# Kernel tuning notes

Hardware: AMD Instinct MI355X
Metric: run time of the kernel (lower is better)

## Reference

```python
import jax, jax.numpy as jnp
import numpy as np
import math

NUM_HEADS = 8
EPS = 1e-12  # torch F.normalize eps


def setup_inputs() -> dict:
    key = jax.random.key(0)
    ks = jax.random.split(key, 11)
    b, t, l, c = 2, 8, 1024, 256
    s = 0.02
    return {
        "q": jax.random.normal(ks[0], (b, t, l, c), jnp.float32),
        "k": jax.random.normal(ks[1], (b, t, l, c), jnp.float32),
        "v": jax.random.normal(ks[2], (b, t, l, c), jnp.float32),
        "Wq": jax.random.normal(ks[3], (c, c), jnp.float32) * s,
        "bq": jax.random.normal(ks[4], (c,), jnp.float32) * s,
        "Wk": jax.random.normal(ks[5], (c, c), jnp.float32) * s,
        "bk": jax.random.normal(ks[6], (c,), jnp.float32) * s,
        "Wv": jax.random.normal(ks[7], (c, c), jnp.float32) * s,
        "bv": jax.random.normal(ks[8], (c,), jnp.float32) * s,
        "Wm": jax.random.normal(ks[9], (c, c), jnp.float32) * s,
        "bm": jax.random.normal(ks[10], (c,), jnp.float32) * s,
    }


def _proj_norm(x, W, bias, h, d):
    # Linear (torch: x @ W.T + b), split heads, L2-normalize over head_dim.
    b_, t_, l_, c_ = x.shape
    y = (x @ W.T + bias).reshape(b_, t_, l_, h, d).transpose(0, 1, 3, 2, 4)  # [b,t,h,l,d]
    n = jnp.maximum(jnp.linalg.norm(y, axis=-1, keepdims=True), EPS)
    return y / n


def reference(q, k, v, Wq, bq, Wk, bk, Wv, bv, Wm, bm):
    b, t, l, c = q.shape
    h = NUM_HEADS
    d = c // h
    shortcut = q
    qn = _proj_norm(q, Wq, bq, h, d)  # [b,t,h,l,d]
    kn = _proj_norm(k, Wk, bk, h, d)
    vn = _proj_norm(v, Wv, bv, h, d)
    scores = jnp.einsum('bthqd,bthkd->bthqk', qn, kn) / math.sqrt(d)
    attn = jax.nn.softmax(scores, axis=-1)
    x = jnp.einsum('bthqk,bthkd->bthqd', attn, vn)  # [b,t,h,l,d]
    x = x.transpose(0, 1, 3, 2, 4).reshape(b, t, l, c)
    return x @ Wm.T + bm + shortcut
```

## Files before the change

### kernel.cpp

```cpp
#include <hip/hip_runtime.h>
#include <hip/hip_bf16.h>


#define NTOK  16384
#define CDIM  256
#define LSEQ  1024
#define HEADS 8
#define DHEAD 32

typedef _Float16 f16;
typedef __attribute__((ext_vector_type(2))) _Float16 f16x2;
typedef __attribute__((ext_vector_type(4))) _Float16 f16x4;
typedef __attribute__((ext_vector_type(8))) _Float16 f16x8;
typedef __attribute__((ext_vector_type(4))) float f32x4;
typedef __attribute__((ext_vector_type(16))) float f32x16;

#define QSCALE (0.17677669529663687f * 1.4426950408889634f)

__device__ __forceinline__ f16x2 pkcvt(float a, float b) {
  auto r = __builtin_amdgcn_cvt_pkrtz(a, b);
  union { decltype(r) in; f16x2 out; } u;
  u.in = r;
  return u.out;
}

__device__ __forceinline__ f16x4 pack4(float4 a) {
  union { f16x4 v; f16x2 h[2]; } u;
  u.h[0] = pkcvt(a.x, a.y);
  u.h[1] = pkcvt(a.z, a.w);
  return u.v;
}

__global__ __launch_bounds__(256)
void cvt_w_kernel(const float* __restrict__ Wq, const float* __restrict__ Wk,
                  const float* __restrict__ Wv, const float* __restrict__ Wm,
                  f16* __restrict__ dst) {
  const int m = blockIdx.x >> 6;
  const float* src = (m == 0) ? Wq : (m == 1) ? Wk : (m == 2) ? Wv : Wm;
  const int base = (blockIdx.x & 63) * 1024 + threadIdx.x * 4;
  const int och = base >> 8, ch = base & 255;
  float4 a = *(const float4*)(src + base);
  *(f16x4*)(dst + m * 65536 + (ch >> 5) * 8192 + och * 32 + (ch & 31)) =
      pack4(a);
}

#define PKKB 1288

__global__ __launch_bounds__(256, 2)
void proj_mfma_kernel(const float* __restrict__ xq, const float* __restrict__ xk,
                      const float* __restrict__ xv, const f16* __restrict__ w16,
                      const float* __restrict__ bq, const float* __restrict__ bk,
                      const float* __restrict__ bv,
                      f16* __restrict__ qn, f16* __restrict__ kn,
                      f16* __restrict__ vt) {
  __shared__ f16 xl[8 * PKKB];
  const int which = blockIdx.y;
  const float* x    = (which == 0) ? xq : (which == 1) ? xk : xv;
  const float* bias = (which == 0) ? bq : (which == 1) ? bk : bv;
  const f16* W      = w16 + which * 65536;
  f16* out          = (which == 0) ? qn : (which == 1) ? kn : vt;
  const float scale = (which == 0) ? QSCALE : 1.0f;
  const bool transposed = (which == 2);

  const int tid = threadIdx.x;
  const int wave = tid >> 6, lane = tid & 63;
  const int quad = lane >> 4, l16 = lane & 15;
  const int tokbase = blockIdx.x * 32;
  const int wbase = wave * 64;

  {
    const int c16 = lane;
#pragma unroll
    for (int r = 0; r < 8; ++r) {
      const int tok = r * 4 + wave;
      float4 a = *(const float4*)(x + (size_t)(tokbase + tok) * CDIM + c16 * 4);
      *(f16x4*)(&xl[(c16 >> 3) * PKKB + tok * 40 + (c16 & 7) * 4]) = pack4(a);
    }
  }
  __syncthreads();

  f32x4 acc[4][2];
#pragma unroll
  for (int mt = 0; mt < 4; ++mt)
#pragma unroll
    for (int nt = 0; nt < 2; ++nt) acc[mt][nt] = (f32x4){0.f, 0.f, 0.f, 0.f};

#pragma unroll
  for (int kk = 0; kk < 8; ++kk) {
    f16x8 af[4];
#pragma unroll
    for (int mt = 0; mt < 4; ++mt)
      af[mt] = *(const f16x8*)(W + kk * 8192 + (wbase + mt * 16 + l16) * 32 +
                               quad * 8);
    f16x8 bf0 = *(const f16x8*)(&xl[kk * PKKB + l16 * 40 + quad * 8]);
    f16x8 bf1 = *(const f16x8*)(&xl[kk * PKKB + (16 + l16) * 40 + quad * 8]);
#pragma unroll
    for (int mt = 0; mt < 4; ++mt) {
      acc[mt][0] = __builtin_amdgcn_mfma_f32_16x16x32_f16(af[mt], bf0,
                                                          acc[mt][0], 0, 0, 0);
      acc[mt][1] = __builtin_amdgcn_mfma_f32_16x16x32_f16(af[mt], bf1,
                                                          acc[mt][1], 0, 0, 0);
    }
  }

  const int bt = tokbase >> 10, l0 = tokbase & 1023;
#pragma unroll
  for (int hh = 0; hh < 2; ++hh) {
    const int h = wave * 2 + hh;
    const size_t hb = (size_t)(bt * HEADS + h) * (LSEQ * DHEAD);
    float4 b0 = *(const float4*)(bias + wbase + hh * 32 + quad * 4);
    float4 b1 = *(const float4*)(bias + wbase + hh * 32 + 16 + quad * 4);
#pragma unroll
    for (int nt = 0; nt < 2; ++nt) {
      f32x4 a0 = acc[hh * 2 + 0][nt];
      f32x4 a1 = acc[hh * 2 + 1][nt];
      float v0[4], v1[4];
      v0[0] = a0[0] + b0.x; v0[1] = a0[1] + b0.y;
      v0[2] = a0[2] + b0.z; v0[3] = a0[3] + b0.w;
      v1[0] = a1[0] + b1.x; v1[1] = a1[1] + b1.y;
      v1[2] = a1[2] + b1.z; v1[3] = a1[3] + b1.w;
      float ss = 0.f;
#pragma unroll
      for (int r = 0; r < 4; ++r) ss += v0[r] * v0[r] + v1[r] * v1[r];
      ss += __shfl_xor(ss, 16);
      ss += __shfl_xor(ss, 32);
      const float inv = scale / fmaxf(sqrtf(ss), 1e-12f);
      const int tok_l = l0 + nt * 16 + l16;
      if (!transposed) {
        f16x4 o0, o1;
#pragma unroll
        for (int r = 0; r < 4; ++r) {
          o0[r] = (f16)(v0[r] * inv);
          o1[r] = (f16)(v1[r] * inv);
        }
        *(f16x4*)(out + hb + (size_t)tok_l * DHEAD + quad * 4) = o0;
        *(f16x4*)(out + hb + (size_t)tok_l * DHEAD + 16 + quad * 4) = o1;
      } else {
        const int tcol = (tok_l & ~12) | ((tok_l & 4) << 1) | ((tok_l & 8) >> 1);
#pragma unroll
        for (int r = 0; r < 4; ++r) {
          out[hb + (size_t)(quad * 4 + r) * LSEQ + tcol] = (f16)(v0[r] * inv);
          out[hb + (size_t)(16 + quad * 4 + r) * LSEQ + tcol] = (f16)(v1[r] * inv);
        }
      }
    }
  }
}

#define TKROW 40
#define TVROW 136

__global__ __launch_bounds__(256, 4)
void attn_mfma_kernel(const f16* __restrict__ qn,
                      const f16* __restrict__ kn,
                      const f16* __restrict__ vt,
                      f16* __restrict__ xo) {
  __shared__ f16 kl[2][128 * TKROW];
  __shared__ f16 vl[2][32 * TVROW];
  const int tid  = threadIdx.x;
  const int wave = tid >> 6, lane = tid & 63;
  const int l32 = lane & 31, hi = lane >> 5;
  const int wid = (blockIdx.x & 7) * 128 + (blockIdx.x >> 3);
  const int bth = wid >> 3;
  const int qbase = ((wid & 7) << 7) + wave * 32;
  const size_t hb = (size_t)bth * (LSEQ * DHEAD);

  const f16* qp = qn + hb + (size_t)(qbase + l32) * DHEAD + hi * 8;
  const f16x8 qf0 = *(const f16x8*)qp;
  const f16x8 qf1 = *(const f16x8*)(qp + 16);

  const int krow_w = wave * 32 + (lane >> 1), kc0 = (lane & 1) * 16;
  const f16* gKb = kn + hb + (size_t)krow_w * DHEAD + kc0;
  const int lK = krow_w * TKROW + kc0;
  const int vrow_w = wave * 8 + (lane >> 3), vc0 = (lane & 7) * 8;
  const f16* gVb = vt + hb + (size_t)vrow_w * LSEQ + vc0;
  const int lV = vrow_w * TVROW + vc0;

  f32x16 oacc, z16;
#pragma unroll
  for (int r = 0; r < 16; ++r) { oacc[r] = 0.f; z16[r] = 0.f; }
  float ls0 = 0.f, ls1 = 0.f;

#define EXPPV(s, v0, v1) { \
    union { f16x8 v; f16x2 h[4]; } _q0, _q1; \
    _Pragma("unroll") \
    for (int i = 0; i < 4; ++i) { \
      float e0 = __builtin_amdgcn_exp2f(s[2 * i]); \
      float e1 = __builtin_amdgcn_exp2f(s[2 * i + 1]); \
      ls0 += e0; ls1 += e1; \
      _q0.h[i] = pkcvt(e0, e1); \
      float e2 = __builtin_amdgcn_exp2f(s[8 + 2 * i]); \
      float e3 = __builtin_amdgcn_exp2f(s[9 + 2 * i]); \
      ls0 += e2; ls1 += e3; \
      _q1.h[i] = pkcvt(e2, e3); \
    } \
    oacc = __builtin_amdgcn_mfma_f32_32x32x16_f16(v0, _q0.v, oacc, 0, 0, 0); \
    oacc = __builtin_amdgcn_mfma_f32_32x32x16_f16(v1, _q1.v, oacc, 0, 0, 0); }

  f16x8 gk0 = *(const f16x8*)gKb;
  f16x8 gk1 = *(const f16x8*)(gKb + 8);
  f16x8 gv0 = *(const f16x8*)gVb;
  f16x8 gv1 = *(const f16x8*)(gVb + 64);
  *(f16x8*)(&kl[0][lK])      = gk0;
  *(f16x8*)(&kl[0][lK + 8])  = gk1;
  *(f16x8*)(&vl[0][lV])      = gv0;
  *(f16x8*)(&vl[0][lV + 64]) = gv1;
  gk0 = *(const f16x8*)(gKb + 128 * DHEAD);
  gk1 = *(const f16x8*)(gKb + 128 * DHEAD + 8);
  gv0 = *(const f16x8*)(gVb + 128);
  gv1 = *(const f16x8*)(gVb + 128 + 64);
  __syncthreads();

  for (int t = 0; t < 8; ++t) {
    const f16* kb = kl[t & 1];
    const f16* vb = vl[t & 1];
    __builtin_amdgcn_s_setprio(1);
#pragma unroll
    for (int sub = 0; sub < 4; ++sub) {
      f16x8 kf0 = *(const f16x8*)(kb + (sub * 32 + l32) * TKROW + hi * 8);
      f16x8 kf1 = *(const f16x8*)(kb + (sub * 32 + l32) * TKROW + hi * 8 + 16);
      f16x8 vf0 = *(const f16x8*)(vb + l32 * TVROW + sub * 32 + hi * 8);
      f16x8 vf1 = *(const f16x8*)(vb + l32 * TVROW + sub * 32 + hi * 8 + 16);
      f32x16 s = __builtin_amdgcn_mfma_f32_32x32x16_f16(kf0, qf0, z16, 0, 0, 0);
      s = __builtin_amdgcn_mfma_f32_32x32x16_f16(kf1, qf1, s, 0, 0, 0);
      EXPPV(s, vf0, vf1)
    }
    __builtin_amdgcn_s_setprio(0);
    if (t < 7) {
      __syncthreads();
      *(f16x8*)(&kl[(t + 1) & 1][lK])      = gk0;
      *(f16x8*)(&kl[(t + 1) & 1][lK + 8])  = gk1;
      *(f16x8*)(&vl[(t + 1) & 1][lV])      = gv0;
      *(f16x8*)(&vl[(t + 1) & 1][lV + 64]) = gv1;
      if (t < 6) {
        gk0 = *(const f16x8*)(gKb + (size_t)(t + 2) * 128 * DHEAD);
        gk1 = *(const f16x8*)(gKb + (size_t)(t + 2) * 128 * DHEAD + 8);
        gv0 = *(const f16x8*)(gVb + (t + 2) * 128);
        gv1 = *(const f16x8*)(gVb + (t + 2) * 128 + 64);
      }
      __syncthreads();
    }
  }
#undef EXPPV

  float lsum = ls0 + ls1;
  lsum += __shfl_xor(lsum, 32);
  const float inv = __builtin_amdgcn_rcpf(lsum);

  f16* op = xo + hb + (size_t)(qbase + l32) * DHEAD + hi * 4;
#pragma unroll
  for (int g = 0; g < 4; ++g) {
    union { f16x4 v; f16x2 h[2]; } o;
    o.h[0] = pkcvt(oacc[4 * g + 0] * inv, oacc[4 * g + 1] * inv);
    o.h[1] = pkcvt(oacc[4 * g + 2] * inv, oacc[4 * g + 3] * inv);
    *(f16x4*)(op + 8 * g) = o.v;
  }
}

#define OKKB 1288

__global__ __launch_bounds__(256, 2)
void out_proj_mfma_kernel(const f16* __restrict__ xatt,
                          const f16* __restrict__ wm16,
                          const float* __restrict__ bm,
                          const float* __restrict__ resid,
                          float* __restrict__ out) {
  __shared__ f16 xl[8 * OKKB];
  const int tid = threadIdx.x;
  const int wave = tid >> 6, lane = tid & 63;
  const int quad = lane >> 4, l16 = lane & 15;
  const int tokbase = blockIdx.x * 32;
  const int wbase = wave * 64;
  const int bt = tokbase >> 10, l0 = tokbase & 1023;

  {
#pragma unroll
    for (int r = 0; r < 4; ++r) {
      const int flat = r * 256 + tid;
      const int kk = flat >> 7, rem = flat & 127;
      const int tok = rem >> 2, c8 = rem & 3;
      const f16* gp = xatt + (size_t)(bt * HEADS + kk) * (LSEQ * DHEAD) +
                      (size_t)(l0 + tok) * DHEAD + c8 * 8;
      *(f16x8*)(&xl[kk * OKKB + tok * 40 + c8 * 8]) = *(const f16x8*)gp;
    }
  }
  __syncthreads();

  f32x4 acc[4][2];
#pragma unroll
  for (int mt = 0; mt < 4; ++mt)
#pragma unroll
    for (int nt = 0; nt < 2; ++nt) acc[mt][nt] = (f32x4){0.f, 0.f, 0.f, 0.f};

#pragma unroll
  for (int kk = 0; kk < 8; ++kk) {
    f16x8 af[4];
#pragma unroll
    for (int mt = 0; mt < 4; ++mt)
      af[mt] = *(const f16x8*)(wm16 + kk * 8192 +
                               (wbase + mt * 16 + l16) * 32 + quad * 8);
    f16x8 bf0 = *(const f16x8*)(&xl[kk * OKKB + l16 * 40 + quad * 8]);
    f16x8 bf1 = *(const f16x8*)(&xl[kk * OKKB + (16 + l16) * 40 + quad * 8]);
#pragma unroll
    for (int mt = 0; mt < 4; ++mt) {
      acc[mt][0] = __builtin_amdgcn_mfma_f32_16x16x32_f16(af[mt], bf0,
                                                          acc[mt][0], 0, 0, 0);
      acc[mt][1] = __builtin_amdgcn_mfma_f32_16x16x32_f16(af[mt], bf1,
                                                          acc[mt][1], 0, 0, 0);
    }
  }

#pragma unroll
  for (int mt = 0; mt < 4; ++mt) {
    float4 bv = *(const float4*)(bm + wbase + mt * 16 + quad * 4);
#pragma unroll
    for (int nt = 0; nt < 2; ++nt) {
      const int tok = tokbase + nt * 16 + l16;
      const size_t off = (size_t)tok * CDIM + wbase + mt * 16 + quad * 4;
      float4 rv = *(const float4*)(resid + off);
      float4 o;
      o.x = acc[mt][nt][0] + bv.x + rv.x;
      o.y = acc[mt][nt][1] + bv.y + rv.y;
      o.z = acc[mt][nt][2] + bv.z + rv.z;
      o.w = acc[mt][nt][3] + bv.w + rv.w;
      *(float4*)(out + off) = o;
    }
  }
}

extern "C" void kernel_launch(void* const* d_in, const int* in_sizes, int n_in,
                              void* d_out, int out_size, void* d_ws,
                              size_t ws_size, hipStream_t stream) {
  const float* q  = (const float*)d_in[0];
  const float* k  = (const float*)d_in[1];
  const float* v  = (const float*)d_in[2];
  const float* Wq = (const float*)d_in[3];
  const float* bq = (const float*)d_in[4];
  const float* Wk = (const float*)d_in[5];
  const float* bk = (const float*)d_in[6];
  const float* Wv = (const float*)d_in[7];
  const float* bv = (const float*)d_in[8];
  const float* Wm = (const float*)d_in[9];
  const float* bm = (const float*)d_in[10];
  float* outp = (float*)d_out;

  f16* ws = (f16*)d_ws;
  const size_t TENS = (size_t)NTOK * CDIM;
  f16* qn  = ws;
  f16* kn  = ws + TENS;
  f16* vt  = ws + 2 * TENS;
  f16* w16 = ws + 3 * TENS;
  f16* xa  = qn;

  dim3 blk(256);
  cvt_w_kernel<<<dim3(256), blk, 0, stream>>>(Wq, Wk, Wv, Wm, w16);
  proj_mfma_kernel<<<dim3(512, 3), blk, 0, stream>>>(q, k, v, w16, bq, bk, bv,
                                                     qn, kn, vt);
  attn_mfma_kernel<<<dim3(1024), blk, 0, stream>>>(qn, kn, vt, xa);
  out_proj_mfma_kernel<<<dim3(512), blk, 0, stream>>>(xa, w16 + 3 * 65536, bm,
                                                      q, outp);
}
```

Before: 155.4 us.

## Process two 32-query tiles per wave in attention to reuse K/V fragments

Each wave in the attention kernel now handles 64 queries as two 32-row tiles that share the same K and V fragments read from LDS. Each block covers 256 queries instead of 128, so the grid is halved and K/V global loads and LDS staging per query drop by half. The cost is a second accumulator set and more registers, so launch bounds drop from 4 to 2 blocks per CU, which lowers occupancy. The grid shrinks to 512 blocks, which may leave CUs less loaded.

After: 157.6 us. About the same (+1.4%).

```diff
diff --git a/kernel.cpp b/kernel.cpp
--- a/kernel.cpp
+++ b/kernel.cpp
@@ -150,7 +150,7 @@
 #define TKROW 40
 #define TVROW 136
 
-__global__ __launch_bounds__(256, 4)
+__global__ __launch_bounds__(256, 2)
 void attn_mfma_kernel(const f16* __restrict__ qn,
                       const f16* __restrict__ kn,
                       const f16* __restrict__ vt,
@@ -160,14 +160,17 @@
   const int tid  = threadIdx.x;
   const int wave = tid >> 6, lane = tid & 63;
   const int l32 = lane & 31, hi = lane >> 5;
-  const int wid = (blockIdx.x & 7) * 128 + (blockIdx.x >> 3);
-  const int bth = wid >> 3;
-  const int qbase = ((wid & 7) << 7) + wave * 32;
+  const int wid = (blockIdx.x & 7) * 64 + (blockIdx.x >> 3);
+  const int bth = wid >> 2;
+  const int qbase = ((wid & 3) << 8) + wave * 64;
   const size_t hb = (size_t)bth * (LSEQ * DHEAD);
 
-  const f16* qp = qn + hb + (size_t)(qbase + l32) * DHEAD + hi * 8;
-  const f16x8 qf0 = *(const f16x8*)qp;
-  const f16x8 qf1 = *(const f16x8*)(qp + 16);
+  const f16* qpA = qn + hb + (size_t)(qbase + l32) * DHEAD + hi * 8;
+  const f16x8 qfA0 = *(const f16x8*)qpA;
+  const f16x8 qfA1 = *(const f16x8*)(qpA + 16);
+  const f16* qpB = qpA + 32 * DHEAD;
+  const f16x8 qfB0 = *(const f16x8*)qpB;
+  const f16x8 qfB1 = *(const f16x8*)(qpB + 16);
 
   const int krow_w = wave * 32 + (lane >> 1), kc0 = (lane & 1) * 16;
   const f16* gKb = kn + hb + (size_t)krow_w * DHEAD + kc0;
@@ -176,22 +179,22 @@
   const f16* gVb = vt + hb + (size_t)vrow_w * LSEQ + vc0;
   const int lV = vrow_w * TVROW + vc0;
 
-  f32x16 oacc, z16;
-#pragma unroll
-  for (int r = 0; r < 16; ++r) { oacc[r] = 0.f; z16[r] = 0.f; }
-  float ls0 = 0.f, ls1 = 0.f;
-
-#define EXPPV(s, v0, v1) { \
+  f32x16 oaccA, oaccB, z16;
+#pragma unroll
+  for (int r = 0; r < 16; ++r) { oaccA[r] = 0.f; oaccB[r] = 0.f; z16[r] = 0.f; }
+  float lsA0 = 0.f, lsA1 = 0.f, lsB0 = 0.f, lsB1 = 0.f;
+
+#define EXPPV(s, v0, v1, oacc, la, lb) { \
     union { f16x8 v; f16x2 h[4]; } _q0, _q1; \
     _Pragma("unroll") \
     for (int i = 0; i < 4; ++i) { \
       float e0 = __builtin_amdgcn_exp2f(s[2 * i]); \
       float e1 = __builtin_amdgcn_exp2f(s[2 * i + 1]); \
-      ls0 += e0; ls1 += e1; \
+      la += e0; lb += e1; \
       _q0.h[i] = pkcvt(e0, e1); \
       float e2 = __builtin_amdgcn_exp2f(s[8 + 2 * i]); \
       float e3 = __builtin_amdgcn_exp2f(s[9 + 2 * i]); \
-      ls0 += e2; ls1 += e3; \
+      la += e2; lb += e3; \
       _q1.h[i] = pkcvt(e2, e3); \
     } \
     oacc = __builtin_amdgcn_mfma_f32_32x32x16_f16(v0, _q0.v, oacc, 0, 0, 0); \
@@ -221,9 +224,12 @@
       f16x8 kf1 = *(const f16x8*)(kb + (sub * 32 + l32) * TKROW + hi * 8 + 16);
       f16x8 vf0 = *(const f16x8*)(vb + l32 * TVROW + sub * 32 + hi * 8);
       f16x8 vf1 = *(const f16x8*)(vb + l32 * TVROW + sub * 32 + hi * 8 + 16);
-      f32x16 s = __builtin_amdgcn_mfma_f32_32x32x16_f16(kf0, qf0, z16, 0, 0, 0);
-      s = __builtin_amdgcn_mfma_f32_32x32x16_f16(kf1, qf1, s, 0, 0, 0);
-      EXPPV(s, vf0, vf1)
+      f32x16 sA = __builtin_amdgcn_mfma_f32_32x32x16_f16(kf0, qfA0, z16, 0, 0, 0);
+      sA = __builtin_amdgcn_mfma_f32_32x32x16_f16(kf1, qfA1, sA, 0, 0, 0);
+      EXPPV(sA, vf0, vf1, oaccA, lsA0, lsA1)
+      f32x16 sB = __builtin_amdgcn_mfma_f32_32x32x16_f16(kf0, qfB0, z16, 0, 0, 0);
+      sB = __builtin_amdgcn_mfma_f32_32x32x16_f16(kf1, qfB1, sB, 0, 0, 0);
+      EXPPV(sB, vf0, vf1, oaccB, lsB0, lsB1)
     }
     __builtin_amdgcn_s_setprio(0);
     if (t < 7) {
@@ -243,17 +249,31 @@
   }
 #undef EXPPV
 
-  float lsum = ls0 + ls1;
-  lsum += __shfl_xor(lsum, 32);
-  const float inv = __builtin_amdgcn_rcpf(lsum);
-
-  f16* op = xo + hb + (size_t)(qbase + l32) * DHEAD + hi * 4;
-#pragma unroll
-  for (int g = 0; g < 4; ++g) {
-    union { f16x4 v; f16x2 h[2]; } o;
-    o.h[0] = pkcvt(oacc[4 * g + 0] * inv, oacc[4 * g + 1] * inv);
-    o.h[1] = pkcvt(oacc[4 * g + 2] * inv, oacc[4 * g + 3] * inv);
-    *(f16x4*)(op + 8 * g) = o.v;
+  {
+    float lsum = lsA0 + lsA1;
+    lsum += __shfl_xor(lsum, 32);
+    const float inv = __builtin_amdgcn_rcpf(lsum);
+    f16* op = xo + hb + (size_t)(qbase + l32) * DHEAD + hi * 4;
+#pragma unroll
+    for (int g = 0; g < 4; ++g) {
+      union { f16x4 v; f16x2 h[2]; } o;
+      o.h[0] = pkcvt(oaccA[4 * g + 0] * inv, oaccA[4 * g + 1] * inv);
+      o.h[1] = pkcvt(oaccA[4 * g + 2] * inv, oaccA[4 * g + 3] * inv);
+      *(f16x4*)(op + 8 * g) = o.v;
+    }
+  }
+  {
+    float lsum = lsB0 + lsB1;
+    lsum += __shfl_xor(lsum, 32);
+    const float inv = __builtin_amdgcn_rcpf(lsum);
+    f16* op = xo + hb + (size_t)(qbase + 32 + l32) * DHEAD + hi * 4;
+#pragma unroll
+    for (int g = 0; g < 4; ++g) {
+      union { f16x4 v; f16x2 h[2]; } o;
+      o.h[0] = pkcvt(oaccB[4 * g + 0] * inv, oaccB[4 * g + 1] * inv);
+      o.h[1] = pkcvt(oaccB[4 * g + 2] * inv, oaccB[4 * g + 3] * inv);
+      *(f16x4*)(op + 8 * g) = o.v;
+    }
   }
 }
 
@@ -356,7 +376,7 @@
   cvt_w_kernel<<<dim3(256), blk, 0, stream>>>(Wq, Wk, Wv, Wm, w16);
   proj_mfma_kernel<<<dim3(512, 3), blk, 0, stream>>>(q, k, v, w16, bq, bk, bv,
                                                      qn, kn, vt);
-  attn_mfma_kernel<<<dim3(1024), blk, 0, stream>>>(qn, kn, vt, xa);
+  attn_mfma_kernel<<<dim3(512), blk, 0, stream>>>(qn, kn, vt, xa);
   out_proj_mfma_kernel<<<dim3(512), blk, 0, stream>>>(xa, w16 + 3 * 65536, bm,
                                                       q, outp);
 }
```
